# Performance work log

Hardware: AMD Instinct MI355X
Metric: run time of the kernel (lower is better)

The kernel has to match this reference:

```python
import jax, jax.numpy as jnp
import numpy as np

N = 100000   # nodes
E = 1000000  # edges
IN = 100     # input feature dim
H = 4        # heads
D = 32       # hidden per head (H*D = 128)
C = 47       # classes
EPS = 1e-5
SLOPE = 0.2  # DGL GATv2 leaky_relu negative slope


def setup_inputs() -> dict:
    key = jax.random.key(0)
    ks = jax.random.split(key, 32)
    lin = lambda k, i, o: (jax.random.normal(k, (i, o), jnp.float32) / np.float32(np.sqrt(i)))
    inp = {}
    inp['x'] = jax.random.normal(ks[0], (N, IN), jnp.float32)
    inp['src'] = jax.random.randint(ks[1], (E,), 0, N, jnp.int32)
    inp['dst'] = jnp.sort(jax.random.randint(ks[2], (E,), 0, N, jnp.int32))
    # layer 0: IN -> H*D, Linear residual (IN != H*D)
    inp['Wsrc0'] = lin(ks[3], IN, H * D); inp['bsrc0'] = jnp.zeros(H * D, jnp.float32)
    inp['Wdst0'] = lin(ks[4], IN, H * D); inp['bdst0'] = jnp.zeros(H * D, jnp.float32)
    inp['attn0'] = lin(ks[5], H, D)
    inp['Wres0'] = lin(ks[6], IN, H * D); inp['bres0'] = jnp.zeros(H * D, jnp.float32)
    # layer 1: H*D -> H*D, Identity residual (128 == 128)
    inp['Wsrc1'] = lin(ks[7], H * D, H * D); inp['bsrc1'] = jnp.zeros(H * D, jnp.float32)
    inp['Wdst1'] = lin(ks[8], H * D, H * D); inp['bdst1'] = jnp.zeros(H * D, jnp.float32)
    inp['attn1'] = lin(ks[9], H, D)
    # layer 2: H*D -> H*C, Linear residual (128 != 188)
    inp['Wsrc2'] = lin(ks[10], H * D, H * C); inp['bsrc2'] = jnp.zeros(H * C, jnp.float32)
    inp['Wdst2'] = lin(ks[11], H * D, H * C); inp['bdst2'] = jnp.zeros(H * C, jnp.float32)
    inp['attn2'] = lin(ks[12], H, C)
    inp['Wres2'] = lin(ks[13], H * D, H * C); inp['bres2'] = jnp.zeros(H * C, jnp.float32)
    # BatchNorm1d params (training-mode batch stats)
    inp['g0'] = jnp.ones(H * D, jnp.float32); inp['be0'] = jnp.zeros(H * D, jnp.float32)
    inp['g1'] = jnp.ones(H * D, jnp.float32); inp['be1'] = jnp.zeros(H * D, jnp.float32)
    return inp


def _gatv2(h, src, dst, Ws, bs, Wd, bd, attn, resval):
    """One GATv2Conv on a full block (src feats == dst feats == h)."""
    Hh, Dd = attn.shape
    fs = (h @ Ws + bs).reshape(-1, Hh, Dd)   # [N,H,D] src projection
    fd = (h @ Wd + bd).reshape(-1, Hh, Dd)   # [N,H,D] dst projection
    e = jax.nn.leaky_relu(fs[src] + fd[dst], SLOPE)         # [E,H,D]
    logits = jnp.einsum('ehd,hd->eh', e, attn)              # [E,H]
    m = jax.ops.segment_max(logits, dst, num_segments=N)    # per-dst max
    ex = jnp.exp(logits - m[dst])
    s = jax.ops.segment_sum(ex, dst, num_segments=N)
    alpha = ex / s[dst]                                      # edge softmax
    out = jax.ops.segment_sum(alpha[:, :, None] * fs[src], dst, num_segments=N)
    return out + resval                                      # [N,H,D]


def _bn(x, g, b):
    mu = x.mean(0)
    v = x.var(0)  # biased, as torch BN training mode
    return g * (x - mu) / jnp.sqrt(v + EPS) + b


def reference(x, src, dst,
              Wsrc0, bsrc0, Wdst0, bdst0, attn0, Wres0, bres0,
              Wsrc1, bsrc1, Wdst1, bdst1, attn1,
              Wsrc2, bsrc2, Wdst2, bdst2, attn2, Wres2, bres2,
              g0, be0, g1, be1):
    # layer 0: conv(+relu activation) -> flatten -> BN -> relu (dropout = eval identity)
    res0 = (x @ Wres0 + bres0).reshape(N, H, D)
    h = jax.nn.relu(_gatv2(x, src, dst, Wsrc0, bsrc0, Wdst0, bdst0, attn0, res0))
    h = jax.nn.relu(_bn(h.reshape(N, H * D), g0, be0))
    # layer 1: Identity residual
    res1 = h.reshape(N, H, D)
    h = jax.nn.relu(_gatv2(h, src, dst, Wsrc1, bsrc1, Wdst1, bdst1, attn1, res1))
    h = jax.nn.relu(_bn(h.reshape(N, H * D), g1, be1))
    # layer 2: no activation; mean over heads; log_softmax
    res2 = (h @ Wres2 + bres2).reshape(N, H, C)
    h = _gatv2(h, src, dst, Wsrc2, bsrc2, Wdst2, bdst2, attn2, res2)
    h = h.mean(1)                                # [N,C]
    return jax.nn.log_softmax(h, axis=-1)
```

## Files before the change

### kernel.cpp

```cpp
#include <hip/hip_runtime.h>
#include <hip/hip_bf16.h>

#define Nn 100000
#define Ee 1000000
#define INF_ 100
#define Hh 4
#define Dd 32
#define HD 128
#define Cc 47
#define HC 188
#define HCP 192
#define PSTR 256
#define EPSV 1e-5f
#define SLOPE 0.2f
#define NBLK ((Nn + 255) / 256)

typedef __hip_bfloat16 bf16;
typedef __attribute__((ext_vector_type(8))) short short8;
typedef __attribute__((ext_vector_type(4))) float f32x4;
typedef __attribute__((ext_vector_type(2))) float f32x2;

__device__ __forceinline__ float tof(bf16 v) { return __bfloat162float(v); }
__device__ __forceinline__ float b2f(unsigned short u) {
    return __uint_as_float((unsigned)u << 16);
}
__device__ __forceinline__ float b2flo(unsigned u) {
    return __uint_as_float(u << 16);
}
__device__ __forceinline__ float b2fhi(unsigned u) {
    return __uint_as_float(u & 0xFFFF0000u);
}
__device__ __forceinline__ float ldb(const bf16* p) {
    return b2f(*(const unsigned short*)p);
}
__device__ __forceinline__ unsigned short f2u(float v) {
    bf16 t = __float2bfloat16(v);
    return *(unsigned short*)&t;
}
__device__ __forceinline__ f32x2 pk2(float x, float y) {
    f32x2 r; r.x = x; r.y = y; return r;
}
__device__ __forceinline__ f32x2 pabs2(f32x2 v) {
    return __builtin_elementwise_max(v, -v);
}
__device__ __forceinline__ f32x2 pfma2(f32x2 a, f32x2 b, f32x2 c) {
    return __builtin_elementwise_fma(a, b, c);
}

template <int C>
__device__ __forceinline__ float dppadd(float v) {
    int m = __builtin_amdgcn_update_dpp(0, __float_as_int(v), C, 0xF, 0xF, false);
    return v + __int_as_float(m);
}
template <int C>
__device__ __forceinline__ float dppmax(float v) {
    int m = __builtin_amdgcn_update_dpp(0, __float_as_int(v), C, 0xF, 0xF, false);
    return fmaxf(v, __int_as_float(m));
}
__device__ __forceinline__ float sum16(float p) {
    p = dppadd<0xB1>(p);
    p = dppadd<0x4E>(p);
    p = dppadd<0x124>(p);
    p = dppadd<0x128>(p);
    return p;
}
__device__ __forceinline__ float max16(float p) {
    p = dppmax<0xB1>(p); p = dppmax<0x4E>(p);
    p = dppmax<0x124>(p); p = dppmax<0x128>(p);
    return p;
}

#define L2E 1.4426950408889634f

__global__ void detect_dtype(const unsigned* __restrict__ x, int* __restrict__ flag) {
    if (blockIdx.x == 0 && threadIdx.x == 0) {
        int good = 0;
        for (int i = 0; i < 256; ++i) {
            unsigned lo = x[i] & 0xFFFFu;
            float v = __uint_as_float(lo << 16);
            float a = fabsf(v);
            if (a > 1e-4f && a < 10.f) good++;
        }
        *flag = (good >= 128) ? 1 : 0;
    }
}

__device__ __forceinline__ float ld_any(const void* p, int i, int isbf) {
    return isbf ? tof(((const bf16*)p)[i]) : ((const float*)p)[i];
}

__global__ void cvt_x(const void* __restrict__ in, bf16* __restrict__ out,
                      const int* __restrict__ flag) {
    int i = blockIdx.x * blockDim.x + threadIdx.x;
    if (i >= Nn * 128) return;
    int row = i >> 7, col = i & 127;
    float v = (col < INF_) ? ld_any(in, row * INF_ + col, *flag) : 0.f;
    out[i] = __float2bfloat16(v);
}

#define NSP 15
struct CvtTab { const void* src[NSP]; int off[NSP + 1]; };

__global__ void cvt_params(CvtTab t, bf16* __restrict__ out, int total,
                           const int* __restrict__ flag) {
    int i = blockIdx.x * blockDim.x + threadIdx.x;
    if (i >= total) return;
    int isbf = *flag;
    int seg = 0;
    while (i >= t.off[seg + 1]) seg++;
    out[i] = __float2bfloat16(ld_any(t.src[seg], i - t.off[seg], isbf));
}

#define WROWS 1280
struct PrepTab { const void* src[8]; int row0[8]; int K[8]; int M[8]; int MP[8]; };

__global__ void prep_all(PrepTab t, bf16* __restrict__ wtb, const int* __restrict__ flag) {
    int i = blockIdx.x * blockDim.x + threadIdx.x;
    if (i >= WROWS * 128) return;
    int row = i >> 7, k = i & 127;
    int isbf = *flag;
    float v = 0.f;
#pragma unroll
    for (int q = 0; q < 8; ++q) {
        if (row >= t.row0[q] && row < t.row0[q] + t.MP[q]) {
            int m = row - t.row0[q];
            if (m < t.M[q] && k < t.K[q])
                v = ld_any(t.src[q], k * t.M[q] + m, isbf);
        }
    }
    wtb[i] = __float2bfloat16(v);
}

__global__ void zero_u32(unsigned* __restrict__ p, int n) {
    int i = blockIdx.x * blockDim.x + threadIdx.x;
    if (i < n) p[i] = 0u;
}

__global__ void src_scale_ptr(const int* __restrict__ src, const int* __restrict__ dst,
                              unsigned* __restrict__ w512, unsigned* __restrict__ w256,
                              int* __restrict__ ptr) {
    int i = blockIdx.x * blockDim.x + threadIdx.x;
    if (i < Ee) {
        unsigned s = (unsigned)src[i];
        w512[i] = s << 9;
        w256[i] = s << 8;
    }
    if (i <= Nn) {
        if (i == Nn) { ptr[Nn] = Ee; return; }
        int lo = 0, hi = Ee;
        while (lo < hi) {
            int mid = (lo + hi) >> 1;
            if (dst[mid] < i) lo = mid + 1; else hi = mid;
        }
        ptr[i] = lo;
    }
}

__global__ void deg_hist_blk(const int* __restrict__ ptr, int* __restrict__ cnt) {
    __shared__ int lh[256];
    int t = threadIdx.x;
    lh[t] = 0;
    __syncthreads();
    int n = blockIdx.x * 256 + t;
    if (n < Nn) {
        int dg = ptr[n + 1] - ptr[n]; if (dg > 255) dg = 255;
        atomicAdd(&lh[dg], 1);
    }
    __syncthreads();
    cnt[blockIdx.x * 256 + t] = lh[t];
}

__global__ void deg_scan_blk(const int* __restrict__ cnt, int* __restrict__ base) {
    __shared__ int totals[256];
    int t = threadIdx.x;
    int s = 0;
    for (int k = 0; k < NBLK; ++k) s += cnt[k * 256 + t];
    totals[t] = s;
    __syncthreads();
    int run = 0;
    for (int b = t + 1; b < 256; ++b) run += totals[b];
    for (int k = 0; k < NBLK; ++k) {
        base[k * 256 + t] = run;
        run += cnt[k * 256 + t];
    }
}

__global__ void deg_scatter_blk(const int* __restrict__ ptr, const int* __restrict__ base,
                                int* __restrict__ perm) {
    __shared__ int lh[256];
    int t = threadIdx.x;
    lh[t] = 0;
    __syncthreads();
    int n = blockIdx.x * 256 + t;
    if (n < Nn) {
        int dg = ptr[n + 1] - ptr[n]; if (dg > 255) dg = 255;
        int loc = atomicAdd(&lh[dg], 1);
        perm[base[blockIdx.x * 256 + dg] + loc] = n;
    }
}

template <int MP, int NOUT, int CS, bool ABN, bool PACK, int OSTR>
__global__ __launch_bounds__(256, 4) void gemm_big(
    const bf16* __restrict__ A, const bf16* __restrict__ Wt,
    const bf16* __restrict__ b0, const bf16* __restrict__ b1,
    const bf16* __restrict__ b2,
    bf16* __restrict__ o0, bf16* __restrict__ o1, bf16* __restrict__ o2,
    int MR, const float* __restrict__ bnp) {
    __shared__ __align__(16) bf16 Al[64 * 136];
    const int row0 = blockIdx.x * 64;
    const int tid = threadIdx.x;
#pragma unroll
    for (int j = 0; j < 4; ++j) {
        int idx = tid + j * 256;
        int r = idx >> 4, kk = (idx & 15) * 8;
        int4 val = {0, 0, 0, 0};
        if (row0 + r < Nn) {
            val = *(const int4*)&A[(size_t)(row0 + r) * 128 + kk];
            if (ABN) {
                short8 av = *(short8*)&val;
                bf16 tmp[8];
#pragma unroll
                for (int u = 0; u < 8; ++u) {
                    float v = b2f((unsigned short)av[u]);
                    v = fmaxf(fmaf(v, bnp[kk + u], bnp[128 + kk + u]), 0.f);
                    tmp[u] = __float2bfloat16(v);
                }
                val = *(int4*)tmp;
            }
        }
        *(int4*)&Al[r * 136 + kk] = val;
    }
    __syncthreads();
    const int wave = tid >> 6, lane = tid & 63;
    const int n16 = lane & 15, quad = lane >> 4;
    const int colbase = blockIdx.y * (64 * CS) + wave * (16 * CS);
    f32x4 acc[4][CS];
#pragma unroll
    for (int rt = 0; rt < 4; ++rt)
#pragma unroll
        for (int c = 0; c < CS; ++c) acc[rt][c] = (f32x4){0.f, 0.f, 0.f, 0.f};
    const bf16* wb[CS];
#pragma unroll
    for (int c = 0; c < CS; ++c)
        wb[c] = Wt + (size_t)(colbase + c * 16 + n16) * 128 + quad * 8;
    const bf16* ap = Al + n16 * 136 + quad * 8;
#pragma unroll
    for (int ks = 0; ks < 4; ++ks) {
        short8 bf[CS];
#pragma unroll
        for (int c = 0; c < CS; ++c) bf[c] = *(const short8*)(wb[c] + ks * 32);
#pragma unroll
        for (int rt = 0; rt < 4; ++rt) {
            short8 af = *(const short8*)(ap + rt * 16 * 136 + ks * 32);
#pragma unroll
            for (int c = 0; c < CS; ++c)
                acc[rt][c] = __builtin_amdgcn_mfma_f32_16x16x32_bf16(af, bf[c], acc[rt][c], 0, 0, 0);
        }
    }
#pragma unroll
    for (int c = 0; c < CS; ++c) {
        int col = colbase + c * 16 + n16;
        int oi = col / MP, lc = col - oi * MP;
        if (oi >= NOUT || lc >= MR) continue;
        const bf16* bp = (oi == 0) ? b0 : (oi == 1) ? b1 : b2;
        bf16* o = (oi == 0) ? o0 : (oi == 1) ? o1 : o2;
        float bb = tof(bp[lc]);
        int st;
        if (PACK) {
            int hh = lc / 47, cc = lc - hh * 47;
            st = ((hh * 16 + (cc & 15)) << 2) + (cc >> 4);
        } else {
            st = lc;
        }
#pragma unroll
        for (int rt = 0; rt < 4; ++rt) {
#pragma unroll
            for (int i = 0; i < 4; ++i) {
                int row = row0 + rt * 16 + quad * 4 + i;
                if (row < Nn)
                    o[(size_t)row * OSTR + st] = __float2bfloat16(acc[rt][c][i] + bb);
            }
        }
    }
}

template <bool RESBN>
__global__ __launch_bounds__(256) void gat_fused_128(
    const bf16* __restrict__ fs, const bf16* __restrict__ fd,
    const unsigned* __restrict__ srcW, const int* __restrict__ ptr,
    const int* __restrict__ perm,
    const bf16* __restrict__ attn, const bf16* __restrict__ resb,
    const float* __restrict__ bnp, bf16* __restrict__ hout) {
    const int wave = threadIdx.x >> 6, lane = threadIdx.x & 63;
    const int di = blockIdx.x * 4 + wave;
    if (di >= Nn) return;
    const int d = perm[di];
    const int c0 = lane * 2;
    const unsigned c0b = (unsigned)c0 * 2u;
    ushort2 aq = *(const ushort2*)&attn[c0];
    float a0 = b2f(aq.x) * L2E, a1 = b2f(aq.y) * L2E;
    const f32x2 Av = pk2(0.6f * a0, 0.6f * a1);
    const f32x2 Bv = pk2(0.4f * a0, 0.4f * a1);
    ushort2 dq = *(const ushort2*)&fd[(size_t)d * HD + c0];
    const f32x2 fdv = pk2(b2f(dq.x), b2f(dq.y));
    const char* fsb = (const char*)fs;
    float l = 0.f;
    f32x2 Ov = pk2(0.f, 0.f);
    int e = ptr[d];
    const int e1 = ptr[d + 1];
    for (; e + 3 < e1; e += 4) {
        unsigned vA = srcW[e] + c0b, vB = srcW[e + 1] + c0b;
        unsigned vC = srcW[e + 2] + c0b, vD = srcW[e + 3] + c0b;
        ushort2 qA = *(const ushort2*)(fsb + vA);
        ushort2 qB = *(const ushort2*)(fsb + vB);
        ushort2 qC = *(const ushort2*)(fsb + vC);
        ushort2 qD = *(const ushort2*)(fsb + vD);
        f32x2 fA = pk2(b2f(qA.x), b2f(qA.y));
        f32x2 fB = pk2(b2f(qB.x), b2f(qB.y));
        f32x2 fC = pk2(b2f(qC.x), b2f(qC.y));
        f32x2 fD = pk2(b2f(qD.x), b2f(qD.y));
        f32x2 xA = fA + fdv, xB = fB + fdv, xC = fC + fdv, xD = fD + fdv;
        f32x2 tA = pfma2(pabs2(xA), Bv, xA * Av);
        f32x2 tB = pfma2(pabs2(xB), Bv, xB * Av);
        f32x2 tC = pfma2(pabs2(xC), Bv, xC * Av);
        f32x2 tD = pfma2(pabs2(xD), Bv, xD * Av);
        float pA = tA.x + tA.y, pB = tB.x + tB.y;
        float pC = tC.x + tC.y, pD = tD.x + tD.y;
        pA = sum16(pA); pB = sum16(pB); pC = sum16(pC); pD = sum16(pD);
        float eA = __builtin_amdgcn_exp2f(pA), eB = __builtin_amdgcn_exp2f(pB);
        float eC = __builtin_amdgcn_exp2f(pC), eD = __builtin_amdgcn_exp2f(pD);
        l += (eA + eB) + (eC + eD);
        Ov = pfma2(pk2(eA, eA), fA, Ov);
        Ov = pfma2(pk2(eB, eB), fB, Ov);
        Ov = pfma2(pk2(eC, eC), fC, Ov);
        Ov = pfma2(pk2(eD, eD), fD, Ov);
    }
    for (; e < e1; ++e) {
        unsigned v = srcW[e] + c0b;
        ushort2 fq = *(const ushort2*)(fsb + v);
        f32x2 f = pk2(b2f(fq.x), b2f(fq.y));
        f32x2 x = f + fdv;
        f32x2 t = pfma2(pabs2(x), Bv, x * Av);
        float p = sum16(t.x + t.y);
        float pe = __builtin_amdgcn_exp2f(p);
        l += pe;
        Ov = pfma2(pk2(pe, pe), f, Ov);
    }
    float inv = l > 0.f ? 1.f / l : 0.f;
    ushort2 rq = *(const ushort2*)&resb[(size_t)d * HD + c0];
    float r0 = b2f(rq.x), r1 = b2f(rq.y);
    if (RESBN) {
        r0 = fmaxf(fmaf(r0, bnp[c0], bnp[HD + c0]), 0.f);
        r1 = fmaxf(fmaf(r1, bnp[c0 + 1], bnp[HD + c0 + 1]), 0.f);
    }
    float v0 = fmaxf(fmaf(Ov.x, inv, r0), 0.f);
    float v1 = fmaxf(fmaf(Ov.y, inv, r1), 0.f);
    ushort2 ov; ov.x = f2u(v0); ov.y = f2u(v1);
    *(ushort2*)&hout[(size_t)d * HD + c0] = ov;
}

__global__ __launch_bounds__(256) void gat_fused_188(
    const bf16* __restrict__ fs, const bf16* __restrict__ fd,
    const unsigned* __restrict__ srcW, const int* __restrict__ ptr,
    const int* __restrict__ perm,
    const bf16* __restrict__ attn, const bf16* __restrict__ rs,
    void* __restrict__ out, const int* __restrict__ flag) {
    const int wave = threadIdx.x >> 6, lane = threadIdx.x & 63;
    const int di = blockIdx.x * 4 + wave;
    if (di >= Nn) return;
    const int d = perm[di];
    const int h = lane >> 4, j = lane & 15;
    const unsigned c0b = (unsigned)lane * 8u;
    const int ca = h * Cc + j;
    const bool has2 = (j < 15);
    float a0 = ldb(&attn[ca]) * L2E;
    float a1 = ldb(&attn[ca + 16]) * L2E;
    float a2 = has2 ? ldb(&attn[ca + 32]) * L2E : 0.f;
    const f32x2 Av = pk2(0.6f * a0, 0.6f * a1);
    const f32x2 Bv = pk2(0.4f * a0, 0.4f * a1);
    const float A2 = 0.6f * a2, B2 = 0.4f * a2;
    const char* fdb = (const char*)fd;
    uint2 dq = *(const uint2*)(fdb + (size_t)d * (PSTR * 2) + c0b);
    const f32x2 fdv = pk2(b2flo(dq.x), b2fhi(dq.x));
    const float fd2 = b2flo(dq.y);
    const char* fsb = (const char*)fs;
    float l = 0.f, O2 = 0.f;
    f32x2 Ov = pk2(0.f, 0.f);
    int e = ptr[d];
    const int e1 = ptr[d + 1];
    for (; e + 3 < e1; e += 4) {
        unsigned vA = srcW[e] + c0b, vB = srcW[e + 1] + c0b;
        unsigned vC = srcW[e + 2] + c0b, vD = srcW[e + 3] + c0b;
        uint2 qA = *(const uint2*)(fsb + vA);
        uint2 qB = *(const uint2*)(fsb + vB);
        uint2 qC = *(const uint2*)(fsb + vC);
        uint2 qD = *(const uint2*)(fsb + vD);
        f32x2 fA = pk2(b2flo(qA.x), b2fhi(qA.x)); float gA = b2flo(qA.y);
        f32x2 fB = pk2(b2flo(qB.x), b2fhi(qB.x)); float gB = b2flo(qB.y);
        f32x2 fC = pk2(b2flo(qC.x), b2fhi(qC.x)); float gC = b2flo(qC.y);
        f32x2 fD = pk2(b2flo(qD.x), b2fhi(qD.x)); float gD = b2flo(qD.y);
        f32x2 xA = fA + fdv, xB = fB + fdv, xC = fC + fdv, xD = fD + fdv;
        float yA = gA + fd2, yB = gB + fd2, yC = gC + fd2, yD = gD + fd2;
        f32x2 tA = pfma2(pabs2(xA), Bv, xA * Av);
        f32x2 tB = pfma2(pabs2(xB), Bv, xB * Av);
        f32x2 tC = pfma2(pabs2(xC), Bv, xC * Av);
        f32x2 tD = pfma2(pabs2(xD), Bv, xD * Av);
        float pA = fmaf(yA, A2, fmaf(fabsf(yA), B2, tA.x + tA.y));
        float pB = fmaf(yB, A2, fmaf(fabsf(yB), B2, tB.x + tB.y));
        float pC = fmaf(yC, A2, fmaf(fabsf(yC), B2, tC.x + tC.y));
        float pD = fmaf(yD, A2, fmaf(fabsf(yD), B2, tD.x + tD.y));
        pA = sum16(pA); pB = sum16(pB); pC = sum16(pC); pD = sum16(pD);
        float eA = __builtin_amdgcn_exp2f(pA), eB = __builtin_amdgcn_exp2f(pB);
        float eC = __builtin_amdgcn_exp2f(pC), eD = __builtin_amdgcn_exp2f(pD);
        l += (eA + eB) + (eC + eD);
        Ov = pfma2(pk2(eA, eA), fA, Ov); O2 = fmaf(eA, gA, O2);
        Ov = pfma2(pk2(eB, eB), fB, Ov); O2 = fmaf(eB, gB, O2);
        Ov = pfma2(pk2(eC, eC), fC, Ov); O2 = fmaf(eC, gC, O2);
        Ov = pfma2(pk2(eD, eD), fD, Ov); O2 = fmaf(eD, gD, O2);
    }
    for (; e < e1; ++e) {
        unsigned v = srcW[e] + c0b;
        uint2 q = *(const uint2*)(fsb + v);
        f32x2 f = pk2(b2flo(q.x), b2fhi(q.x)); float g = b2flo(q.y);
        f32x2 x = f + fdv;
        float y = g + fd2;
        f32x2 t = pfma2(pabs2(x), Bv, x * Av);
        float p = fmaf(y, A2, fmaf(fabsf(y), B2, t.x + t.y));
        p = sum16(p);
        float pe = __builtin_amdgcn_exp2f(p);
        l += pe;
        Ov = pfma2(pk2(pe, pe), f, Ov); O2 = fmaf(pe, g, O2);
    }
    float inv = l > 0.f ? 1.f / l : 0.f;
    const char* rb_ = (const char*)rs;
    uint2 rq = *(const uint2*)(rb_ + (size_t)d * (PSTR * 2) + c0b);
    float v0 = fmaf(Ov.x, inv, b2flo(rq.x));
    float v1 = fmaf(Ov.y, inv, b2fhi(rq.x));
    float v2 = has2 ? fmaf(O2, inv, b2flo(rq.y)) : 0.f;
    v0 += __shfl_xor(v0, 16); v0 += __shfl_xor(v0, 32); v0 *= 0.25f;
    v1 += __shfl_xor(v1, 16); v1 += __shfl_xor(v1, 32); v1 *= 0.25f;
    v2 += __shfl_xor(v2, 16); v2 += __shfl_xor(v2, 32); v2 *= 0.25f;
    float mx = fmaxf(v0, v1);
    if (has2) mx = fmaxf(mx, v2);
    mx = max16(mx);
    float sm = __expf(v0 - mx) + __expf(v1 - mx) + (has2 ? __expf(v2 - mx) : 0.f);
    sm = sum16(sm);
    if (h == 0) {
        float ls = mx + logf(sm);
        if (*flag) {
            bf16* o = (bf16*)out + (size_t)d * Cc;
            o[j] = __float2bfloat16(v0 - ls);
            o[j + 16] = __float2bfloat16(v1 - ls);
            if (has2) o[j + 32] = __float2bfloat16(v2 - ls);
        } else {
            float* o = (float*)out + (size_t)d * Cc;
            o[j] = v0 - ls;
            o[j + 16] = v1 - ls;
            if (has2) o[j + 32] = v2 - ls;
        }
    }
}

__global__ void col_stats(const bf16* __restrict__ in, float* __restrict__ sums) {
    int c = threadIdx.x;
    int r0 = blockIdx.x * 256;
    int r1 = r0 + 256; if (r1 > Nn) r1 = Nn;
    float s = 0.f, s2 = 0.f;
    for (int r = r0; r < r1; ++r) {
        float v = ldb(&in[(size_t)r * HD + c]);
        s += v; s2 += v * v;
    }
    atomicAdd(&sums[c], s);
    atomicAdd(&sums[HD + c], s2);
}

__global__ void bn_finalize(const float* __restrict__ sums, const bf16* __restrict__ g,
                            const bf16* __restrict__ be, float* __restrict__ ss) {
    int c = threadIdx.x;
    float mu = sums[c] * (1.f / Nn);
    float var = sums[HD + c] * (1.f / Nn) - mu * mu;
    float sc = tof(g[c]) * rsqrtf(var + EPSV);
    ss[c] = sc;
    ss[HD + c] = tof(be[c]) - mu * sc;
}

extern "C" void kernel_launch(void* const* d_in, const int* in_sizes, int n_in,
                              void* d_out, int out_size, void* d_ws, size_t ws_size,
                              hipStream_t stream) {
    (void)in_sizes; (void)n_in; (void)out_size; (void)ws_size;
    const void* x = d_in[0];
    const int* src = (const int*)d_in[1];
    const int* dst = (const int*)d_in[2];

    char* ws = (char*)d_ws;
    size_t off = 0;
    auto alloc = [&](size_t bytes) {
        void* p = ws + off;
        off += (bytes + 255) & ~(size_t)255;
        return p;
    };
    bf16* xb = (bf16*)alloc((size_t)Nn * 128 * 2);
    bf16* rb = (bf16*)alloc((size_t)Nn * HD * 2);
    bf16* rs = xb;
    bf16* fs = (bf16*)alloc((size_t)Nn * HCP * 2);
    bf16* fd = (bf16*)alloc((size_t)Nn * HCP * 2);
    bf16* hbA = (bf16*)alloc((size_t)Nn * HD * 2);
    bf16* hbB = (bf16*)alloc((size_t)Nn * HD * 2);
    bf16* fs2 = fs;
    bf16* fd2 = fs + (size_t)Nn * PSTR;
    int* ptr = (int*)alloc((Nn + 1) * 4);
    bf16* wtb = (bf16*)alloc((size_t)WROWS * 128 * 2);
    float* bns = (float*)alloc(2 * HD * 4);
    float* bnss0 = (float*)alloc(2 * HD * 4);
    float* bnss1 = (float*)alloc(2 * HD * 4);
    bf16* pb = (bf16*)alloc(4096 * 2);
    int* flag = (int*)alloc(256);
    unsigned* w512 = (unsigned*)alloc((size_t)Ee * 4);
    unsigned* w256 = (unsigned*)alloc((size_t)Ee * 4);
    int* cnt = (int*)alloc((size_t)256 * NBLK * 4);
    int* cbase = (int*)alloc((size_t)256 * NBLK * 4);
    int* perm = (int*)alloc((size_t)Nn * 4);

    static const int spIdx[NSP] = {4, 6, 7, 9, 11, 13, 14, 16, 18, 19, 21, 22, 23, 24, 25};
    static const int spSz[NSP]  = {HD, HD, HD, HD, HD, HD, HD, HC, HC, HC, HC, HD, HD, HD, HD};
    CvtTab tab;
    int tot = 0;
    for (int i = 0; i < NSP; ++i) { tab.src[i] = d_in[spIdx[i]]; tab.off[i] = tot; tot += spSz[i]; }
    tab.off[NSP] = tot;
    const bf16 *bsrc0 = pb + tab.off[0], *bdst0 = pb + tab.off[1], *attn0 = pb + tab.off[2],
               *bres0 = pb + tab.off[3], *bsrc1 = pb + tab.off[4], *bdst1 = pb + tab.off[5],
               *attn1 = pb + tab.off[6], *bsrc2 = pb + tab.off[7], *bdst2 = pb + tab.off[8],
               *attn2 = pb + tab.off[9], *bres2 = pb + tab.off[10],
               *g0 = pb + tab.off[11], *be0 = pb + tab.off[12],
               *g1 = pb + tab.off[13], *be1 = pb + tab.off[14];

    PrepTab pt;
    static const int wIdx[8] = {3, 5, 8, 10, 12, 15, 17, 20};
    static const int wK[8]   = {INF_, INF_, INF_, HD, HD, HD, HD, HD};
    static const int wM[8]   = {HD, HD, HD, HD, HD, HC, HC, HC};
    static const int wMP[8]  = {128, 128, 128, 128, 128, 192, 192, 192};
    static const int wR0[8]  = {0, 128, 256, 384, 512, 640, 832, 1024};
    for (int i = 0; i < 8; ++i) {
        pt.src[i] = d_in[wIdx[i]]; pt.row0[i] = wR0[i];
        pt.K[i] = wK[i]; pt.M[i] = wM[i]; pt.MP[i] = wMP[i];
    }

    detect_dtype<<<1, 64, 0, stream>>>((const unsigned*)x, flag);
    cvt_x<<<(Nn * 128 + 255) / 256, 256, 0, stream>>>(x, xb, flag);
    cvt_params<<<(tot + 255) / 256, 256, 0, stream>>>(tab, pb, tot, flag);
    prep_all<<<(WROWS * 128 + 255) / 256, 256, 0, stream>>>(pt, wtb, flag);
    src_scale_ptr<<<(Ee + 255) / 256, 256, 0, stream>>>(src, dst, w512, w256, ptr);
    deg_hist_blk<<<NBLK, 256, 0, stream>>>(ptr, cnt);
    deg_scan_blk<<<1, 256, 0, stream>>>(cnt, cbase);
    deg_scatter_blk<<<NBLK, 256, 0, stream>>>(ptr, cbase, perm);

    const int fusedGrid = (Nn + 3) / 4;
    const int statsGrid = NBLK;
    const int rowBlk = (Nn + 63) / 64;

    gemm_big<128, 3, 3, false, false, HD><<<dim3(rowBlk, 2), 256, 0, stream>>>(
        xb, wtb, bsrc0, bdst0, bres0, fs, fd, rb, HD, nullptr);
    gat_fused_128<false><<<fusedGrid, 256, 0, stream>>>(fs, fd, w256, ptr, perm,
                                                        attn0, rb, nullptr, hbA);
    zero_u32<<<1, 256, 0, stream>>>((unsigned*)bns, 2 * HD);
    col_stats<<<statsGrid, 128, 0, stream>>>(hbA, bns);
    bn_finalize<<<1, HD, 0, stream>>>(bns, g0, be0, bnss0);

    gemm_big<128, 2, 2, true, false, HD><<<dim3(rowBlk, 2), 256, 0, stream>>>(
        hbA, wtb + (size_t)384 * 128, bsrc1, bdst1, nullptr, fs, fd, nullptr, HD, bnss0);
    gat_fused_128<true><<<fusedGrid, 256, 0, stream>>>(fs, fd, w256, ptr, perm,
                                                       attn1, hbA, bnss0, hbB);
    zero_u32<<<1, 256, 0, stream>>>((unsigned*)bns, 2 * HD);
    col_stats<<<statsGrid, 128, 0, stream>>>(hbB, bns);
    bn_finalize<<<1, HD, 0, stream>>>(bns, g1, be1, bnss1);

    gemm_big<192, 3, 3, true, true, PSTR><<<dim3(rowBlk, 3), 256, 0, stream>>>(
        hbB, wtb + (size_t)640 * 128, bsrc2, bdst2, bres2, fs2, fd2, rs, HC, bnss1);
    gat_fused_188<<<fusedGrid, 256, 0, stream>>>(fs2, fd2, w512, ptr, perm, attn2, rs,
                                                 d_out, flag);
}
```

Measured before the change: 715.6 us.

## Compact layer-2 feature rows to 192 columns and parallelize degree scan

Layer-2 projected features move from a padded 256-column layout with interleaved (4 per lane) packing to a 192-column layout. Each row is split into a 2-element-per-lane region and a 1-element-per-lane tail, which cuts the bytes gathered per edge and the memory footprint. Each gather becomes a 4-byte plus a 2-byte load instead of one 8-byte load. Separately, the single-block serial degree-bucket scan is replaced by two multi-block wave-parallel kernels using a transposed count layout, at the cost of one extra launch.

```diff
diff --git a/kernel.cpp b/kernel.cpp
--- a/kernel.cpp
+++ b/kernel.cpp
@@ -10,7 +10,6 @@
 #define Cc 47
 #define HC 188
 #define HCP 192
-#define PSTR 256
 #define EPSV 1e-5f
 #define SLOPE 0.2f
 #define NBLK ((Nn + 255) / 256)
@@ -137,12 +136,12 @@
 }
 
 __global__ void src_scale_ptr(const int* __restrict__ src, const int* __restrict__ dst,
-                              unsigned* __restrict__ w512, unsigned* __restrict__ w256,
+                              unsigned* __restrict__ w384, unsigned* __restrict__ w256,
                               int* __restrict__ ptr) {
     int i = blockIdx.x * blockDim.x + threadIdx.x;
     if (i < Ee) {
         unsigned s = (unsigned)src[i];
-        w512[i] = s << 9;
+        w384[i] = s * 384u;
         w256[i] = s << 8;
     }
     if (i <= Nn) {
@@ -167,21 +166,39 @@
         atomicAdd(&lh[dg], 1);
     }
     __syncthreads();
-    cnt[blockIdx.x * 256 + t] = lh[t];
-}
-
-__global__ void deg_scan_blk(const int* __restrict__ cnt, int* __restrict__ base) {
-    __shared__ int totals[256];
-    int t = threadIdx.x;
+    cnt[t * NBLK + blockIdx.x] = lh[t];
+}
+
+__global__ void deg_totals(const int* __restrict__ cnt, int* __restrict__ totals) {
+    int wave = threadIdx.x >> 6, lane = threadIdx.x & 63;
+    int bin = blockIdx.x * 4 + wave;
     int s = 0;
-    for (int k = 0; k < NBLK; ++k) s += cnt[k * 256 + t];
-    totals[t] = s;
-    __syncthreads();
-    int run = 0;
-    for (int b = t + 1; b < 256; ++b) run += totals[b];
-    for (int k = 0; k < NBLK; ++k) {
-        base[k * 256 + t] = run;
-        run += cnt[k * 256 + t];
+    for (int k = lane; k < NBLK; k += 64) s += cnt[bin * NBLK + k];
+#pragma unroll
+    for (int o = 1; o < 64; o <<= 1) s += __shfl_xor(s, o);
+    if (lane == 0) totals[bin] = s;
+}
+
+__global__ void deg_bases(const int* __restrict__ cnt, const int* __restrict__ totals,
+                          int* __restrict__ base) {
+    int wave = threadIdx.x >> 6, lane = threadIdx.x & 63;
+    int bin = blockIdx.x * 4 + wave;
+    int bb = 0;
+    for (int b = bin + 1 + lane; b < 256; b += 64) bb += totals[b];
+#pragma unroll
+    for (int o = 1; o < 64; o <<= 1) bb += __shfl_xor(bb, o);
+    int run = bb;
+    for (int k0 = 0; k0 < NBLK; k0 += 64) {
+        int k = k0 + lane;
+        int c = (k < NBLK) ? cnt[bin * NBLK + k] : 0;
+        int p = c;
+#pragma unroll
+        for (int o = 1; o < 64; o <<= 1) {
+            int t = __shfl_up(p, o);
+            if (lane >= o) p += t;
+        }
+        if (k < NBLK) base[bin * NBLK + k] = run + (p - c);
+        run += __shfl(p, 63);
     }
 }
 
@@ -195,7 +212,7 @@
     if (n < Nn) {
         int dg = ptr[n + 1] - ptr[n]; if (dg > 255) dg = 255;
         int loc = atomicAdd(&lh[dg], 1);
-        perm[base[blockIdx.x * 256 + dg] + loc] = n;
+        perm[base[dg * NBLK + blockIdx.x] + loc] = n;
     }
 }
 
@@ -268,7 +285,9 @@
         int st;
         if (PACK) {
             int hh = lc / 47, cc = lc - hh * 47;
-            st = ((hh * 16 + (cc & 15)) << 2) + (cc >> 4);
+            int jj = cc & 15, kk2 = cc >> 4;
+            int l = hh * 16 + jj;
+            st = (kk2 < 2) ? (2 * l + kk2) : (128 + l);
         } else {
             st = lc;
         }
@@ -370,7 +389,8 @@
     if (di >= Nn) return;
     const int d = perm[di];
     const int h = lane >> 4, j = lane & 15;
-    const unsigned c0b = (unsigned)lane * 8u;
+    const unsigned cbA = (unsigned)lane * 4u;
+    const unsigned cbB = 256u + (unsigned)lane * 2u;
     const int ca = h * Cc + j;
     const bool has2 = (j < 15);
     float a0 = ldb(&attn[ca]) * L2E;
@@ -380,25 +400,30 @@
     const f32x2 Bv = pk2(0.4f * a0, 0.4f * a1);
     const float A2 = 0.6f * a2, B2 = 0.4f * a2;
     const char* fdb = (const char*)fd;
-    uint2 dq = *(const uint2*)(fdb + (size_t)d * (PSTR * 2) + c0b);
-    const f32x2 fdv = pk2(b2flo(dq.x), b2fhi(dq.x));
-    const float fd2 = b2flo(dq.y);
+    const size_t drow = (size_t)d * 384u;
+    unsigned dqa = *(const unsigned*)(fdb + drow + cbA);
+    unsigned short dqb = *(const unsigned short*)(fdb + drow + cbB);
+    const f32x2 fdv = pk2(b2flo(dqa), b2fhi(dqa));
+    const float fd2 = b2f(dqb);
     const char* fsb = (const char*)fs;
     float l = 0.f, O2 = 0.f;
     f32x2 Ov = pk2(0.f, 0.f);
     int e = ptr[d];
     const int e1 = ptr[d + 1];
     for (; e + 3 < e1; e += 4) {
-        unsigned vA = srcW[e] + c0b, vB = srcW[e + 1] + c0b;
-        unsigned vC = srcW[e + 2] + c0b, vD = srcW[e + 3] + c0b;
-        uint2 qA = *(const uint2*)(fsb + vA);
-        uint2 qB = *(const uint2*)(fsb + vB);
-        uint2 qC = *(const uint2*)(fsb + vC);
-        uint2 qD = *(const uint2*)(fsb + vD);
-        f32x2 fA = pk2(b2flo(qA.x), b2fhi(qA.x)); float gA = b2flo(qA.y);
-        f32x2 fB = pk2(b2flo(qB.x), b2fhi(qB.x)); float gB = b2flo(qB.y);
-        f32x2 fC = pk2(b2flo(qC.x), b2fhi(qC.x)); float gC = b2flo(qC.y);
-        f32x2 fD = pk2(b2flo(qD.x), b2fhi(qD.x)); float gD = b2flo(qD.y);
+        unsigned bA = srcW[e], bB = srcW[e + 1], bC = srcW[e + 2], bD = srcW[e + 3];
+        unsigned qA = *(const unsigned*)(fsb + bA + cbA);
+        unsigned qB = *(const unsigned*)(fsb + bB + cbA);
+        unsigned qC = *(const unsigned*)(fsb + bC + cbA);
+        unsigned qD = *(const unsigned*)(fsb + bD + cbA);
+        unsigned short uA = *(const unsigned short*)(fsb + bA + cbB);
+        unsigned short uB = *(const unsigned short*)(fsb + bB + cbB);
+        unsigned short uC = *(const unsigned short*)(fsb + bC + cbB);
+        unsigned short uD = *(const unsigned short*)(fsb + bD + cbB);
+        f32x2 fA = pk2(b2flo(qA), b2fhi(qA)); float gA = b2f(uA);
+        f32x2 fB = pk2(b2flo(qB), b2fhi(qB)); float gB = b2f(uB);
+        f32x2 fC = pk2(b2flo(qC), b2fhi(qC)); float gC = b2f(uC);
+        f32x2 fD = pk2(b2flo(qD), b2fhi(qD)); float gD = b2f(uD);
         f32x2 xA = fA + fdv, xB = fB + fdv, xC = fC + fdv, xD = fD + fdv;
         float yA = gA + fd2, yB = gB + fd2, yC = gC + fd2, yD = gD + fd2;
         f32x2 tA = pfma2(pabs2(xA), Bv, xA * Av);
@@ -419,9 +444,10 @@
         Ov = pfma2(pk2(eD, eD), fD, Ov); O2 = fmaf(eD, gD, O2);
     }
     for (; e < e1; ++e) {
-        unsigned v = srcW[e] + c0b;
-        uint2 q = *(const uint2*)(fsb + v);
-        f32x2 f = pk2(b2flo(q.x), b2fhi(q.x)); float g = b2flo(q.y);
+        unsigned b = srcW[e];
+        unsigned q = *(const unsigned*)(fsb + b + cbA);
+        unsigned short u = *(const unsigned short*)(fsb + b + cbB);
+        f32x2 f = pk2(b2flo(q), b2fhi(q)); float g = b2f(u);
         f32x2 x = f + fdv;
         float y = g + fd2;
         f32x2 t = pfma2(pabs2(x), Bv, x * Av);
@@ -433,10 +459,11 @@
     }
     float inv = l > 0.f ? 1.f / l : 0.f;
     const char* rb_ = (const char*)rs;
-    uint2 rq = *(const uint2*)(rb_ + (size_t)d * (PSTR * 2) + c0b);
-    float v0 = fmaf(Ov.x, inv, b2flo(rq.x));
-    float v1 = fmaf(Ov.y, inv, b2fhi(rq.x));
-    float v2 = has2 ? fmaf(O2, inv, b2flo(rq.y)) : 0.f;
+    unsigned rqa = *(const unsigned*)(rb_ + drow + cbA);
+    unsigned short rqb = *(const unsigned short*)(rb_ + drow + cbB);
+    float v0 = fmaf(Ov.x, inv, b2flo(rqa));
+    float v1 = fmaf(Ov.y, inv, b2fhi(rqa));
+    float v2 = has2 ? fmaf(O2, inv, b2f(rqb)) : 0.f;
     v0 += __shfl_xor(v0, 16); v0 += __shfl_xor(v0, 32); v0 *= 0.25f;
     v1 += __shfl_xor(v1, 16); v1 += __shfl_xor(v1, 32); v1 *= 0.25f;
     v2 += __shfl_xor(v2, 16); v2 += __shfl_xor(v2, 32); v2 *= 0.25f;
@@ -506,8 +533,6 @@
     bf16* fd = (bf16*)alloc((size_t)Nn * HCP * 2);
     bf16* hbA = (bf16*)alloc((size_t)Nn * HD * 2);
     bf16* hbB = (bf16*)alloc((size_t)Nn * HD * 2);
-    bf16* fs2 = fs;
-    bf16* fd2 = fs + (size_t)Nn * PSTR;
     int* ptr = (int*)alloc((Nn + 1) * 4);
     bf16* wtb = (bf16*)alloc((size_t)WROWS * 128 * 2);
     float* bns = (float*)alloc(2 * HD * 4);
@@ -515,10 +540,11 @@
     float* bnss1 = (float*)alloc(2 * HD * 4);
     bf16* pb = (bf16*)alloc(4096 * 2);
     int* flag = (int*)alloc(256);
-    unsigned* w512 = (unsigned*)alloc((size_t)Ee * 4);
+    unsigned* w384 = (unsigned*)alloc((size_t)Ee * 4);
     unsigned* w256 = (unsigned*)alloc((size_t)Ee * 4);
     int* cnt = (int*)alloc((size_t)256 * NBLK * 4);
     int* cbase = (int*)alloc((size_t)256 * NBLK * 4);
+    int* totals = (int*)alloc(256 * 4);
     int* perm = (int*)alloc((size_t)Nn * 4);
 
     static const int spIdx[NSP] = {4, 6, 7, 9, 11, 13, 14, 16, 18, 19, 21, 22, 23, 24, 25};
@@ -549,9 +575,10 @@
     cvt_x<<<(Nn * 128 + 255) / 256, 256, 0, stream>>>(x, xb, flag);
     cvt_params<<<(tot + 255) / 256, 256, 0, stream>>>(tab, pb, tot, flag);
     prep_all<<<(WROWS * 128 + 255) / 256, 256, 0, stream>>>(pt, wtb, flag);
-    src_scale_ptr<<<(Ee + 255) / 256, 256, 0, stream>>>(src, dst, w512, w256, ptr);
+    src_scale_ptr<<<(Ee + 255) / 256, 256, 0, stream>>>(src, dst, w384, w256, ptr);
     deg_hist_blk<<<NBLK, 256, 0, stream>>>(ptr, cnt);
-    deg_scan_blk<<<1, 256, 0, stream>>>(cnt, cbase);
+    deg_totals<<<64, 256, 0, stream>>>(cnt, totals);
+    deg_bases<<<64, 256, 0, stream>>>(cnt, totals, cbase);
     deg_scatter_blk<<<NBLK, 256, 0, stream>>>(ptr, cbase, perm);
 
     const int fusedGrid = (Nn + 3) / 4;
@@ -574,8 +601,8 @@
     col_stats<<<statsGrid, 128, 0, stream>>>(hbB, bns);
     bn_finalize<<<1, HD, 0, stream>>>(bns, g1, be1, bnss1);
 
-    gemm_big<192, 3, 3, true, true, PSTR><<<dim3(rowBlk, 3), 256, 0, stream>>>(
-        hbB, wtb + (size_t)640 * 128, bsrc2, bdst2, bres2, fs2, fd2, rs, HC, bnss1);
-    gat_fused_188<<<fusedGrid, 256, 0, stream>>>(fs2, fd2, w512, ptr, perm, attn2, rs,
+    gemm_big<192, 3, 3, true, true, HCP><<<dim3(rowBlk, 3), 256, 0, stream>>>(
+        hbB, wtb + (size_t)640 * 128, bsrc2, bdst2, bres2, fs, fd, rs, HC, bnss1);
+    gat_fused_188<<<fusedGrid, 256, 0, stream>>>(fs, fd, w384, ptr, perm, attn2, rs,
                                                  d_out, flag);
 }
```

New measurement: 663.9 us. -7.2%, faster.
